# Kernel optimization log

Measured on AMD Instinct MI355X. Metric: run time of the kernel, lower is better.

The kernel has to match this reference:

```python
import jax, jax.numpy as jnp
import numpy as np

C = 2.0 + 1e-6
_nodes, _weights = np.polynomial.laguerre.laggauss(2)
QUAD_NODES = jnp.asarray(np.maximum(_nodes, 0.01) / C, dtype=jnp.float32)
QUAD_WEIGHTS = jnp.asarray(np.maximum(_weights, 0.01) / C, dtype=jnp.float32)
H, HD, P, M = 4, 64, 16, 32  # heads, head_dim, poly_dim, num_features
NUM_LABELS = 131072


def safe_normalize(x, axis=-1, eps=1e-4):
    n = jnp.linalg.norm(x, axis=axis, keepdims=True)
    return x / jnp.maximum(n, eps)


def safe_log(x, eps=1e-8):
    return jnp.log(jnp.maximum(x, eps))


def slay_features(x, omega, anchors):
    # x: [N, H*HD]; omega: [R,H,HD,M] (pre-scaled); anchors: [P,HD] (unit-norm)
    N = x.shape[0]
    xr = safe_normalize(x.reshape(N, H, HD), axis=-1)
    poly_proj = jnp.clip(jnp.einsum('nhd,pd->nhp', xr, anchors), -1.0, 1.0)
    poly_feat = poly_proj ** 2 / np.float32(np.sqrt(P))          # [N,H,P]
    prf_proj = jnp.einsum('nhd,rhdm->rnhm', xr, omega)           # [R,N,H,M]
    s = jnp.maximum(QUAD_NODES, 1e-6).reshape(-1, 1, 1, 1)
    exp_arg = jnp.clip(prf_proj * jnp.sqrt(2.0 * s) - s, -20.0, 20.0)
    prf_feat = jnp.exp(exp_arg) / np.float32(np.sqrt(M + 1e-6))
    prf_feat = prf_feat * jnp.sqrt(jnp.maximum(QUAD_WEIGHTS, 1e-6)).reshape(-1, 1, 1, 1)
    # fuse poly x prf, concat over quadrature nodes r (r-major feature order)
    fused = poly_feat[None, :, :, :, None] * prf_feat[:, :, :, None, :]  # [R,N,H,P,M]
    return fused.transpose(1, 0, 2, 3, 4).reshape(N, -1)         # [N, R*H*P*M]


def setup_inputs() -> dict:
    key = jax.random.key(0)
    ks = jax.random.split(key, 9)
    B, L, K = 1024, 128, 8
    return {
        'indices': jax.random.randint(ks[0], (B, L), 0, 100000),
        'mask': jnp.ones((B, L), dtype=jnp.float32),
        'labels': jax.random.randint(ks[1], (B, K), 0, NUM_LABELS),
        'label_mask': jnp.ones((B, K), dtype=jnp.float32),
        'neg_indices': jax.random.randint(ks[2], (2048,), 0, NUM_LABELS),
        'embed_table': jax.random.normal(ks[3], (100000, 256), dtype=jnp.float32),
        'kernel': jax.random.normal(ks[4], (256, NUM_LABELS), dtype=jnp.float32),
        'omega': jax.random.normal(ks[5], (2, H, HD, M), dtype=jnp.float32),
        'anchors': jax.random.normal(ks[6], (P, HD), dtype=jnp.float32),
    }


def reference(indices, mask, labels, label_mask, neg_indices, embed_table, kernel, omega, anchors):
    B, K = labels.shape
    # init-time parameter normalizations from the module
    omega_n = omega / np.float32(np.sqrt(HD))
    anchors_n = anchors / jnp.linalg.norm(anchors, axis=-1, keepdims=True)
    # MeanEmbedding encoder
    embeds = embed_table[indices]                                 # [B,L,D]
    summed = jnp.sum(embeds * mask[:, :, None], axis=1)
    query = summed / jnp.maximum(jnp.sum(mask, axis=1, keepdims=True), 1.0)
    query = safe_normalize(query, axis=-1)
    phi_query = slay_features(query, omega_n, anchors_n)          # [B,F]
    # sampled classifier rows
    W = safe_normalize(kernel.T, axis=-1)                         # [num_labels,D]
    safe_labels = jnp.maximum(labels, 0)
    all_needed = jnp.concatenate([safe_labels.reshape(-1), neg_indices])  # [B*K+Nneg]
    W_subset = W[all_needed]
    phi_W = slay_features(W_subset, omega_n, anchors_n)           # [B*K+Nneg,F]
    scores = phi_query @ phi_W.T                                  # [B, B*K+Nneg]
    idx_offsets = jnp.arange(B)[:, None] * K + jnp.arange(K)[None, :]
    pos_scores = jnp.take_along_axis(scores, idx_offsets, axis=1) # [B,K]
    neg_scores = scores[:, B * K:]                                # [B,Nneg]
    all_scores = jnp.concatenate([pos_scores, neg_scores], axis=1) + 1e-8
    log_Z = jax.scipy.special.logsumexp(safe_log(all_scores), axis=1)
    log_probs = safe_log(pos_scores + 1e-8) - log_Z[:, None]
    return -jnp.sum(log_probs * label_mask) / (jnp.sum(label_mask) + 1e-6)
```

## Files before the change

kernel.cpp:

```cpp
#include <hip/hip_runtime.h>
#include <math.h>

#define B_Q 1024
#define L_SEQ 128
#define D_EMB 256
#define NLAB 131072
#define LBL_ROWS 8192
#define NEG_ROWS 2048
#define W_ROWS 10240
#define CROW 320
#define RPB 32
#define SXS 258
#define QST 84
#define NWT 32

__device__ __forceinline__ float wave_sum(float v) {
#pragma unroll
  for (int off = 32; off > 0; off >>= 1) v += __shfl_xor(v, off, 64);
  return v;
}

__device__ __forceinline__ void slay_tail(const float* __restrict__ sx, int t,
                                          const float* __restrict__ anchT,
                                          const float* __restrict__ omega,
                                          float* __restrict__ outrow) {
  if (t < 64) {
    const int h = t >> 4, p = t & 15;
    const float* x = sx + h * 64;
    float d = 0.f;
#pragma unroll
    for (int dd = 0; dd < 64; dd++) d = fmaf(x[dd], anchT[dd * 16 + p], d);
    d = fminf(fmaxf(d, -1.0f), 1.0f);
    outrow[h * 16 + p] = d * d * 0.25f;
  }
  {
    const int r = t >> 7;
    const int h = (t >> 5) & 3;
    const float* x = sx + h * 64;
    const float* om = omega + (size_t)(t >> 5) * 2048 + (t & 31);
    float d = 0.f;
#pragma unroll
    for (int dd = 0; dd < 64; dd++) d = fmaf(x[dd], om[dd * 32], d);
    const float proj = d * 0.125f;
    const float s = r ? 1.70710592763316f : 0.29289307236691f;
    const float w = r ? 0.07322326809171f : 0.42677648190829f;
    float arg = proj * sqrtf(2.0f * s) - s;
    arg = fminf(fmaxf(arg, -20.0f), 20.0f);
    outrow[64 + t] = expf(arg) * (sqrtf(w) / sqrtf(32.000001f));
  }
}

__global__ __launch_bounds__(256) void k_setup(const float* __restrict__ anchors,
                                               const int* __restrict__ labels,
                                               const int* __restrict__ negidx,
                                               float* __restrict__ anchT,
                                               int* __restrict__ jidx,
                                               int* __restrict__ sorted) {
  __shared__ int shist[2048];
  __shared__ int s2[256];
  const int t = threadIdx.x, bx = blockIdx.x;
  if (bx == 0) {
    if (t < 64) {
      for (int p = 0; p < 16; p++) {
        const float v = anchors[p * 64 + t];
        const float n = sqrtf(wave_sum(v * v));
        anchT[t * 16 + p] = v / n;
      }
    }
  } else {
    for (int i = t; i < 2048; i += 256) shist[i] = 0;
    __syncthreads();
    int4 lv[8], nv[2];
#pragma unroll
    for (int e = 0; e < 8; e++) {
      int4 v = ((const int4*)labels)[e * 256 + t];
      v.x = max(v.x, 0); v.y = max(v.y, 0); v.z = max(v.z, 0); v.w = max(v.w, 0);
      lv[e] = v;
      ((int4*)jidx)[e * 256 + t] = v;
      atomicAdd(&shist[v.x >> 6], 1); atomicAdd(&shist[v.y >> 6], 1);
      atomicAdd(&shist[v.z >> 6], 1); atomicAdd(&shist[v.w >> 6], 1);
    }
#pragma unroll
    for (int e = 0; e < 2; e++) {
      const int4 v = ((const int4*)negidx)[e * 256 + t];
      nv[e] = v;
      ((int4*)jidx)[2048 + e * 256 + t] = v;
      atomicAdd(&shist[v.x >> 6], 1); atomicAdd(&shist[v.y >> 6], 1);
      atomicAdd(&shist[v.z >> 6], 1); atomicAdd(&shist[v.w >> 6], 1);
    }
    __syncthreads();
    int v[8]; int sum = 0;
#pragma unroll
    for (int e = 0; e < 8; e++) { v[e] = shist[t * 8 + e]; sum += v[e]; }
    s2[t] = sum; __syncthreads();
    for (int off = 1; off < 256; off <<= 1) {
      const int x = s2[t];
      const int y = (t >= off) ? s2[t - off] : 0;
      __syncthreads();
      s2[t] = x + y;
      __syncthreads();
    }
    int run = s2[t] - sum;
#pragma unroll
    for (int e = 0; e < 8; e++) { shist[t * 8 + e] = run; run += v[e]; }
    __syncthreads();
#pragma unroll
    for (int e = 0; e < 8; e++) {
      const int i = (e * 256 + t) * 4;
      sorted[atomicAdd(&shist[lv[e].x >> 6], 1)] = i;
      sorted[atomicAdd(&shist[lv[e].y >> 6], 1)] = i + 1;
      sorted[atomicAdd(&shist[lv[e].z >> 6], 1)] = i + 2;
      sorted[atomicAdd(&shist[lv[e].w >> 6], 1)] = i + 3;
    }
#pragma unroll
    for (int e = 0; e < 2; e++) {
      const int i = LBL_ROWS + (e * 256 + t) * 4;
      sorted[atomicAdd(&shist[nv[e].x >> 6], 1)] = i;
      sorted[atomicAdd(&shist[nv[e].y >> 6], 1)] = i + 1;
      sorted[atomicAdd(&shist[nv[e].z >> 6], 1)] = i + 2;
      sorted[atomicAdd(&shist[nv[e].w >> 6], 1)] = i + 3;
    }
  }
}

__global__ __launch_bounds__(256, 4) void k_feat(const int* __restrict__ indices,
                                                 const float* __restrict__ mask,
                                                 const float* __restrict__ embed,
                                                 const float* __restrict__ kern,
                                                 const float* __restrict__ anchT,
                                                 const float* __restrict__ omega,
                                                 const int* __restrict__ jidx,
                                                 const int* __restrict__ sorted,
                                                 float* __restrict__ qcomp,
                                                 float* __restrict__ wcomp) {
  __shared__ __align__(16) float smem[9504];
  const int tid = threadIdx.x;

  if (blockIdx.x < B_Q) {
    const int b = blockIdx.x, t = tid;
    const int wv = t >> 6, ln = t & 63;
    int* sidx = (int*)smem;
    float* smask = smem + 128;
    float4* spart = (float4*)(smem + 256);
    float* smsum = smem + 1280;
    float* sx = smem + 1296;
    if (t < L_SEQ) { sidx[t] = indices[b * L_SEQ + t]; smask[t] = mask[b * L_SEQ + t]; }
    __syncthreads();
    float4 acc = {0.f, 0.f, 0.f, 0.f};
    float msum = 0.f;
#pragma unroll 8
    for (int l = wv * 32; l < wv * 32 + 32; l++) {
      const float m = smask[l];
      msum += m;
      const float4 e = *(const float4*)(embed + (size_t)sidx[l] * D_EMB + ln * 4);
      acc.x = fmaf(e.x, m, acc.x); acc.y = fmaf(e.y, m, acc.y);
      acc.z = fmaf(e.z, m, acc.z); acc.w = fmaf(e.w, m, acc.w);
    }
    spart[wv * 64 + ln] = acc;
    if (ln == 0) smsum[wv] = msum;
    __syncthreads();
    const float* spf = (const float*)spart;
    float q = spf[t] + spf[256 + t] + spf[512 + t] + spf[768 + t];
    const float mt = smsum[0] + smsum[1] + smsum[2] + smsum[3];
    q /= fmaxf(mt, 1.0f);
    const float ss = wave_sum(q * q);
    sx[t] = q / fmaxf(sqrtf(ss), 1e-4f);
    __syncthreads();
    slay_tail(sx, t, anchT, omega, qcomp + (size_t)b * CROW);
  } else {
    const int lb = blockIdx.x - B_Q;
    int* sj = (int*)smem;
    int* ssid = (int*)smem + 32;
    float* rnorm = smem + 64;
    float* sq = smem + 192;
    float* sx = smem + 1248;
    const int cb = (lb & 7) * 40 + (lb >> 3);
    const int i0 = cb * RPB;

    if (tid < RPB) {
      const int sid = sorted[i0 + tid];
      ssid[tid] = sid;
      sj[tid] = jidx[sid];
    }
    __syncthreads();

    {
      const int row = tid & 31, dloc = tid >> 5;
      const float* kbase = kern + ((size_t)dloc << 17) + (size_t)sj[row];
      float ssq[4] = {0.f, 0.f, 0.f, 0.f};
#pragma unroll
      for (int it = 0; it < 32; it++) {
        const float v = kbase[(size_t)it << 20];
        sx[row * SXS + it * 8 + dloc] = v;
        ssq[it >> 3] = fmaf(v, v, ssq[it >> 3]);
      }
#pragma unroll
      for (int h = 0; h < 4; h++) sq[row * 33 + dloc * 4 + h] = ssq[h];
    }
    __syncthreads();
    if (tid < 128) {
      const int r2 = tid >> 2, h = tid & 3;
      float s = 0.f;
#pragma unroll
      for (int dl = 0; dl < 8; dl++) s += sq[r2 * 33 + dl * 4 + h];
      rnorm[r2 * 4 + h] = 1.0f / fmaxf(sqrtf(s), 1e-4f);
    }
    __syncthreads();

    {
      const int hh = (tid >> 5) & 3, r = tid >> 7;
      const float* om = omega + (size_t)(tid >> 5) * 2048 + (tid & 31);
      const float s = r ? 1.70710592763316f : 0.29289307236691f;
      const float w = r ? 0.07322326809171f : 0.42677648190829f;
      const float sc = sqrtf(2.0f * s);
      const float outs = sqrtf(w) / sqrtf(32.000001f);
#pragma unroll
      for (int half = 0; half < 2; half++) {
        float acc[16];
#pragma unroll
        for (int rq = 0; rq < 16; rq++) acc[rq] = 0.f;
#pragma unroll
        for (int dd = 0; dd < 64; dd += 2) {
          const float o0 = om[dd * 32], o1 = om[dd * 32 + 32];
#pragma unroll
          for (int rq = 0; rq < 16; rq++) {
            const float2 xv = *(const float2*)(sx + (half * 16 + rq) * SXS + hh * 64 + dd);
            acc[rq] = fmaf(xv.x, o0, fmaf(xv.y, o1, acc[rq]));
          }
        }
#pragma unroll
        for (int rq = 0; rq < 16; rq++) {
          const int row = half * 16 + rq;
          float arg = acc[rq] * 0.125f * rnorm[row * 4 + hh] * sc - s;
          arg = fminf(fmaxf(arg, -20.0f), 20.0f);
          wcomp[(size_t)ssid[row] * CROW + 64 + tid] = expf(arg) * outs;
        }
      }
    }

    {
      const int hp = tid & 63, rp = tid >> 6;
      const int h = hp >> 4, p = hp & 15;
#pragma unroll
      for (int pr = 0; pr < 4; pr++) {
        const int r0 = rp * 8 + pr * 2;
        const float* x0 = sx + r0 * SXS + h * 64;
        const float* x1 = x0 + SXS;
        float d0 = 0.f, d1 = 0.f;
#pragma unroll
        for (int dd = 0; dd < 64; dd++) {
          const float a = anchT[dd * 16 + p];
          d0 = fmaf(x0[dd], a, d0);
          d1 = fmaf(x1[dd], a, d1);
        }
        d0 *= rnorm[r0 * 4 + h];
        d1 *= rnorm[(r0 + 1) * 4 + h];
        d0 = fminf(fmaxf(d0, -1.0f), 1.0f);
        d1 = fminf(fmaxf(d1, -1.0f), 1.0f);
        wcomp[(size_t)ssid[r0] * CROW + h * 16 + p]     = d0 * d0 * 0.25f;
        wcomp[(size_t)ssid[r0 + 1] * CROW + h * 16 + p] = d1 * d1 * 0.25f;
      }
    }
  }
}

__global__ __launch_bounds__(256) void k_score(const float* __restrict__ qcomp,
                                               const float* __restrict__ wcomp,
                                               float* __restrict__ negparts,
                                               float* __restrict__ pos) {
  __shared__ __align__(16) float sq[128 * QST];
  __shared__ __align__(16) float swt[80 * 64];
  const int tid = threadIdx.x;

  if (blockIdx.x < 256) {
    const int qt = blockIdx.x & 7;
    const int wb = blockIdx.x >> 3;
    const int q0 = qt * 128;
    const int wr0 = LBL_ROWS + wb * 64;
    const int qg = tid >> 4;
    const int wg = tid & 15;

    float acc[8][4];
#pragma unroll
    for (int i = 0; i < 8; i++)
#pragma unroll
      for (int j = 0; j < 4; j++) acc[i][j] = 0.f;

    for (int h = 0; h < 4; h++) {
#pragma unroll
      for (int k = 0; k < 10; k++) {
        const int idx = k * 256 + tid;
        const int row = idx / 20, c4 = idx % 20;
        int col;
        if (c4 < 4)       col = h * 16 + c4 * 4;
        else if (c4 < 12) col = 64 + h * 32 + (c4 - 4) * 4;
        else              col = 192 + h * 32 + (c4 - 12) * 4;
        const float4 v = *(const float4*)(qcomp + (size_t)(q0 + row) * CROW + col);
        *(float4*)(sq + row * QST + c4 * 4) = v;
      }
#pragma unroll
      for (int k = 0; k < 5; k++) {
        const int idx = k * 256 + tid;
        const int row = idx / 20, c4 = idx % 20;
        int col;
        if (c4 < 4)       col = h * 16 + c4 * 4;
        else if (c4 < 12) col = 64 + h * 32 + (c4 - 4) * 4;
        else              col = 192 + h * 32 + (c4 - 12) * 4;
        const float4 v = *(const float4*)(wcomp + (size_t)(wr0 + row) * CROW + col);
        swt[(c4 * 4 + 0) * 64 + row] = v.x;
        swt[(c4 * 4 + 1) * 64 + row] = v.y;
        swt[(c4 * 4 + 2) * 64 + row] = v.z;
        swt[(c4 * 4 + 3) * 64 + row] = v.w;
      }
      __syncthreads();

      float pd[8][4], pf[8][4];
#pragma unroll
      for (int i = 0; i < 8; i++)
#pragma unroll
        for (int j = 0; j < 4; j++) { pd[i][j] = 0.f; pf[i][j] = 0.f; }

#pragma unroll
      for (int c = 0; c < 20; c++) {
        float4 qv[8];
#pragma unroll
        for (int i = 0; i < 8; i++)
          qv[i] = *(const float4*)(sq + (qg * 8 + i) * QST + c * 4);
#pragma unroll
        for (int k = 0; k < 4; k++) {
          const float4 wvk = *(const float4*)(swt + (c * 4 + k) * 64 + wg * 4);
          if (c < 4) {
#pragma unroll
            for (int i = 0; i < 8; i++) {
              const float qik = ((const float*)&qv[i])[k];
              pd[i][0] = fmaf(qik, wvk.x, pd[i][0]);
              pd[i][1] = fmaf(qik, wvk.y, pd[i][1]);
              pd[i][2] = fmaf(qik, wvk.z, pd[i][2]);
              pd[i][3] = fmaf(qik, wvk.w, pd[i][3]);
            }
          } else {
#pragma unroll
            for (int i = 0; i < 8; i++) {
              const float qik = ((const float*)&qv[i])[k];
              pf[i][0] = fmaf(qik, wvk.x, pf[i][0]);
              pf[i][1] = fmaf(qik, wvk.y, pf[i][1]);
              pf[i][2] = fmaf(qik, wvk.z, pf[i][2]);
              pf[i][3] = fmaf(qik, wvk.w, pf[i][3]);
            }
          }
        }
      }
#pragma unroll
      for (int i = 0; i < 8; i++)
#pragma unroll
        for (int j = 0; j < 4; j++) acc[i][j] = fmaf(pd[i][j], pf[i][j], acc[i][j]);
      __syncthreads();
    }

#pragma unroll
    for (int i = 0; i < 8; i++) {
      float r = acc[i][0] + acc[i][1] + acc[i][2] + acc[i][3];
      r += __shfl_xor(r, 1, 64);
      r += __shfl_xor(r, 2, 64);
      r += __shfl_xor(r, 4, 64);
      r += __shfl_xor(r, 8, 64);
      if (wg == 0) negparts[wb * B_Q + q0 + qg * 8 + i] = r;
    }
  } else {
    const int g = (blockIdx.x - 256) * 64 + (tid >> 2);
    const int h = tid & 3;
    const float* q = qcomp + (size_t)(g >> 3) * CROW;
    const float* w = wcomp + (size_t)g * CROW;
    float pd = 0.f, pf = 0.f;
#pragma unroll
    for (int c = 0; c < 4; c++) {
      const float4 qv = *(const float4*)(q + h * 16 + c * 4);
      const float4 wv = *(const float4*)(w + h * 16 + c * 4);
      pd += qv.x * wv.x + qv.y * wv.y + qv.z * wv.z + qv.w * wv.w;
    }
#pragma unroll
    for (int r = 0; r < 2; r++)
#pragma unroll
      for (int c = 0; c < 8; c++) {
        const float4 qv = *(const float4*)(q + 64 + r * 128 + h * 32 + c * 4);
        const float4 wv = *(const float4*)(w + 64 + r * 128 + h * 32 + c * 4);
        pf += qv.x * wv.x + qv.y * wv.y + qv.z * wv.z + qv.w * wv.w;
      }
    float sc = pd * pf;
    sc += __shfl_xor(sc, 1, 64);
    sc += __shfl_xor(sc, 2, 64);
    if (h == 0) pos[g] = sc;
  }
}

__global__ __launch_bounds__(1024) void k_loss(const float* __restrict__ pos,
                                               const float* __restrict__ negparts,
                                               const float* __restrict__ lmask,
                                               float* __restrict__ out) {
  const int b = threadIdx.x;
  float lp[8];
  float possum = 0.f;
#pragma unroll
  for (int k = 0; k < 8; k++) { lp[k] = pos[b * 8 + k]; possum += lp[k]; }
  float negsum = 0.f;
#pragma unroll 8
  for (int c = 0; c < NWT; c++) negsum += negparts[c * B_Q + b];
  const float Z = possum + negsum + 2.056e-5f;
  const float logZ = logf(Z);
  float local = 0.f, lsum = 0.f;
#pragma unroll
  for (int k = 0; k < 8; k++) {
    const float lm = lmask[b * 8 + k];
    local += lm * (logf(lp[k] + 1e-8f) - logZ);
    lsum += lm;
  }
  local = wave_sum(local);
  lsum = wave_sum(lsum);
  __shared__ float r1[16], r2[16];
  const int wid = b >> 6;
  if ((b & 63) == 0) { r1[wid] = local; r2[wid] = lsum; }
  __syncthreads();
  if (b == 0) {
    float t1 = 0.f, t2 = 0.f;
    for (int wv = 0; wv < 16; wv++) { t1 += r1[wv]; t2 += r2[wv]; }
    out[0] = -t1 / (t2 + 1e-6f);
  }
}

extern "C" void kernel_launch(void* const* d_in, const int* in_sizes, int n_in,
                              void* d_out, int out_size, void* d_ws, size_t ws_size,
                              hipStream_t stream) {
  const int* indices  = (const int*)d_in[0];
  const float* mask   = (const float*)d_in[1];
  const int* labels   = (const int*)d_in[2];
  const float* lmask  = (const float*)d_in[3];
  const int* negidx   = (const int*)d_in[4];
  const float* embed  = (const float*)d_in[5];
  const float* kern   = (const float*)d_in[6];
  const float* omega  = (const float*)d_in[7];
  const float* anchors= (const float*)d_in[8];
  float* out = (float*)d_out;

  float* ws = (float*)d_ws;
  float* anchT    = ws;
  float* qcomp    = anchT + 1024;
  float* wcomp    = qcomp + (size_t)B_Q * CROW;
  float* pos      = wcomp + (size_t)W_ROWS * CROW;
  float* negparts = pos + LBL_ROWS;
  int*   jidx     = (int*)(negparts + NWT * B_Q);
  int*   sorted   = jidx + W_ROWS;

  k_setup<<<2, 256, 0, stream>>>(anchors, labels, negidx, anchT, jidx, sorted);
  k_feat<<<B_Q + W_ROWS / RPB, 256, 0, stream>>>(indices, mask, embed, kern, anchT, omega,
                                                 jidx, sorted, qcomp, wcomp);
  k_score<<<256 + 128, 256, 0, stream>>>(qcomp, wcomp, negparts, pos);
  k_loss<<<1, 1024, 0, stream>>>(pos, negparts, lmask, out);
}
```

Measured before the change: 357.1 us.

## Shrink W-feature blocks to 8 rows and schedule them before query blocks

The classifier-row feature path now processes 8 gathered rows per block instead of 32, giving 1280 smaller blocks with far less shared memory. Each thread loads one embedding dimension for all 8 rows, and row norms come from wave reductions instead of a shared partial-sum pass. The W blocks are also launched ahead of the query-embedding blocks. The aim is higher occupancy and more memory parallelism for the strided column gather from the kernel matrix. The cost is that the omega and anchor loads are reused across fewer rows per block.

```diff
diff --git a/kernel.cpp b/kernel.cpp
--- a/kernel.cpp
+++ b/kernel.cpp
@@ -9,7 +9,8 @@
 #define NEG_ROWS 2048
 #define W_ROWS 10240
 #define CROW 320
-#define RPB 32
+#define RPB 8
+#define NWB 1280
 #define SXS 258
 #define QST 84
 #define NWT 32
@@ -123,21 +124,98 @@
   }
 }
 
-__global__ __launch_bounds__(256, 4) void k_feat(const int* __restrict__ indices,
-                                                 const float* __restrict__ mask,
-                                                 const float* __restrict__ embed,
-                                                 const float* __restrict__ kern,
-                                                 const float* __restrict__ anchT,
-                                                 const float* __restrict__ omega,
-                                                 const int* __restrict__ jidx,
-                                                 const int* __restrict__ sorted,
-                                                 float* __restrict__ qcomp,
-                                                 float* __restrict__ wcomp) {
-  __shared__ __align__(16) float smem[9504];
+__global__ __launch_bounds__(256) void k_feat(const int* __restrict__ indices,
+                                              const float* __restrict__ mask,
+                                              const float* __restrict__ embed,
+                                              const float* __restrict__ kern,
+                                              const float* __restrict__ anchT,
+                                              const float* __restrict__ omega,
+                                              const int* __restrict__ jidx,
+                                              const int* __restrict__ sorted,
+                                              float* __restrict__ qcomp,
+                                              float* __restrict__ wcomp) {
+  __shared__ __align__(16) float smem[2112];
   const int tid = threadIdx.x;
 
-  if (blockIdx.x < B_Q) {
-    const int b = blockIdx.x, t = tid;
+  if (blockIdx.x < NWB) {
+    const int lb = blockIdx.x;
+    int* sj = (int*)smem;
+    int* ssid = (int*)smem + 8;
+    float* rnorm = smem + 16;
+    float* sx = smem + 48;
+    const int cb = (lb & 7) * 160 + (lb >> 3);
+    const int i0 = cb * RPB;
+
+    if (tid < RPB) {
+      const int sid = sorted[i0 + tid];
+      ssid[tid] = sid;
+      sj[tid] = jidx[sid];
+    }
+    __syncthreads();
+
+    {
+      const float* kbase = kern + ((size_t)tid << 17);
+      float vv[8];
+#pragma unroll
+      for (int k = 0; k < RPB; k++) vv[k] = kbase[sj[k]];
+#pragma unroll
+      for (int k = 0; k < RPB; k++) {
+        sx[k * SXS + tid] = vv[k];
+        const float ss = wave_sum(vv[k] * vv[k]);
+        if ((tid & 63) == 0) rnorm[k * 4 + (tid >> 6)] = 1.0f / fmaxf(sqrtf(ss), 1e-4f);
+      }
+    }
+    __syncthreads();
+
+    {
+      const int hh = (tid >> 5) & 3, r = tid >> 7;
+      const float* om = omega + (size_t)(tid >> 5) * 2048 + (tid & 31);
+      const float s = r ? 1.70710592763316f : 0.29289307236691f;
+      const float w = r ? 0.07322326809171f : 0.42677648190829f;
+      const float sc = sqrtf(2.0f * s);
+      const float outs = sqrtf(w) / sqrtf(32.000001f);
+      float acc[RPB];
+#pragma unroll
+      for (int k = 0; k < RPB; k++) acc[k] = 0.f;
+#pragma unroll
+      for (int dd = 0; dd < 64; dd += 2) {
+        const float o0 = om[dd * 32], o1 = om[dd * 32 + 32];
+#pragma unroll
+        for (int k = 0; k < RPB; k++) {
+          const float2 xv = *(const float2*)(sx + k * SXS + hh * 64 + dd);
+          acc[k] = fmaf(xv.x, o0, fmaf(xv.y, o1, acc[k]));
+        }
+      }
+#pragma unroll
+      for (int k = 0; k < RPB; k++) {
+        float arg = acc[k] * 0.125f * rnorm[k * 4 + hh] * sc - s;
+        arg = fminf(fmaxf(arg, -20.0f), 20.0f);
+        wcomp[(size_t)ssid[k] * CROW + 64 + tid] = expf(arg) * outs;
+      }
+    }
+
+    {
+      const int hp = tid & 63, rp = tid >> 6;
+      const int h = hp >> 4, p = hp & 15;
+      const int r0 = rp * 2;
+      const float* x0 = sx + r0 * SXS + h * 64;
+      const float* x1 = x0 + SXS;
+      float d0 = 0.f, d1 = 0.f;
+#pragma unroll
+      for (int dd = 0; dd < 64; dd++) {
+        const float a = anchT[dd * 16 + p];
+        d0 = fmaf(x0[dd], a, d0);
+        d1 = fmaf(x1[dd], a, d1);
+      }
+      d0 *= rnorm[r0 * 4 + h];
+      d1 *= rnorm[(r0 + 1) * 4 + h];
+      d0 = fminf(fmaxf(d0, -1.0f), 1.0f);
+      d1 = fminf(fmaxf(d1, -1.0f), 1.0f);
+      wcomp[(size_t)ssid[r0] * CROW + h * 16 + p]     = d0 * d0 * 0.25f;
+      wcomp[(size_t)ssid[r0 + 1] * CROW + h * 16 + p] = d1 * d1 * 0.25f;
+    }
+  } else {
+    const int b = blockIdx.x - NWB, t = tid;
     const int wv = t >> 6, ln = t & 63;
     int* sidx = (int*)smem;
     float* smask = smem + 128;
@@ -167,100 +245,6 @@
     sx[t] = q / fmaxf(sqrtf(ss), 1e-4f);
     __syncthreads();
     slay_tail(sx, t, anchT, omega, qcomp + (size_t)b * CROW);
-  } else {
-    const int lb = blockIdx.x - B_Q;
-    int* sj = (int*)smem;
-    int* ssid = (int*)smem + 32;
-    float* rnorm = smem + 64;
-    float* sq = smem + 192;
-    float* sx = smem + 1248;
-    const int cb = (lb & 7) * 40 + (lb >> 3);
-    const int i0 = cb * RPB;
-
-    if (tid < RPB) {
-      const int sid = sorted[i0 + tid];
-      ssid[tid] = sid;
-      sj[tid] = jidx[sid];
-    }
-    __syncthreads();
-
-    {
-      const int row = tid & 31, dloc = tid >> 5;
-      const float* kbase = kern + ((size_t)dloc << 17) + (size_t)sj[row];
-      float ssq[4] = {0.f, 0.f, 0.f, 0.f};
-#pragma unroll
-      for (int it = 0; it < 32; it++) {
-        const float v = kbase[(size_t)it << 20];
-        sx[row * SXS + it * 8 + dloc] = v;
-        ssq[it >> 3] = fmaf(v, v, ssq[it >> 3]);
-      }
-#pragma unroll
-      for (int h = 0; h < 4; h++) sq[row * 33 + dloc * 4 + h] = ssq[h];
-    }
-    __syncthreads();
-    if (tid < 128) {
-      const int r2 = tid >> 2, h = tid & 3;
-      float s = 0.f;
-#pragma unroll
-      for (int dl = 0; dl < 8; dl++) s += sq[r2 * 33 + dl * 4 + h];
-      rnorm[r2 * 4 + h] = 1.0f / fmaxf(sqrtf(s), 1e-4f);
-    }
-    __syncthreads();
-
-    {
-      const int hh = (tid >> 5) & 3, r = tid >> 7;
-      const float* om = omega + (size_t)(tid >> 5) * 2048 + (tid & 31);
-      const float s = r ? 1.70710592763316f : 0.29289307236691f;
-      const float w = r ? 0.07322326809171f : 0.42677648190829f;
-      const float sc = sqrtf(2.0f * s);
-      const float outs = sqrtf(w) / sqrtf(32.000001f);
-#pragma unroll
-      for (int half = 0; half < 2; half++) {
-        float acc[16];
-#pragma unroll
-        for (int rq = 0; rq < 16; rq++) acc[rq] = 0.f;
-#pragma unroll
-        for (int dd = 0; dd < 64; dd += 2) {
-          const float o0 = om[dd * 32], o1 = om[dd * 32 + 32];
-#pragma unroll
-          for (int rq = 0; rq < 16; rq++) {
-            const float2 xv = *(const float2*)(sx + (half * 16 + rq) * SXS + hh * 64 + dd);
-            acc[rq] = fmaf(xv.x, o0, fmaf(xv.y, o1, acc[rq]));
-          }
-        }
-#pragma unroll
-        for (int rq = 0; rq < 16; rq++) {
-          const int row = half * 16 + rq;
-          float arg = acc[rq] * 0.125f * rnorm[row * 4 + hh] * sc - s;
-          arg = fminf(fmaxf(arg, -20.0f), 20.0f);
-          wcomp[(size_t)ssid[row] * CROW + 64 + tid] = expf(arg) * outs;
-        }
-      }
-    }
-
-    {
-      const int hp = tid & 63, rp = tid >> 6;
-      const int h = hp >> 4, p = hp & 15;
-#pragma unroll
-      for (int pr = 0; pr < 4; pr++) {
-        const int r0 = rp * 8 + pr * 2;
-        const float* x0 = sx + r0 * SXS + h * 64;
-        const float* x1 = x0 + SXS;
-        float d0 = 0.f, d1 = 0.f;
-#pragma unroll
-        for (int dd = 0; dd < 64; dd++) {
-          const float a = anchT[dd * 16 + p];
-          d0 = fmaf(x0[dd], a, d0);
-          d1 = fmaf(x1[dd], a, d1);
-        }
-        d0 *= rnorm[r0 * 4 + h];
-        d1 *= rnorm[(r0 + 1) * 4 + h];
-        d0 = fminf(fmaxf(d0, -1.0f), 1.0f);
-        d1 = fminf(fmaxf(d1, -1.0f), 1.0f);
-        wcomp[(size_t)ssid[r0] * CROW + h * 16 + p]     = d0 * d0 * 0.25f;
-        wcomp[(size_t)ssid[r0 + 1] * CROW + h * 16 + p] = d1 * d1 * 0.25f;
-      }
-    }
   }
 }
 
@@ -451,8 +435,8 @@
   int*   sorted   = jidx + W_ROWS;
 
   k_setup<<<2, 256, 0, stream>>>(anchors, labels, negidx, anchT, jidx, sorted);
-  k_feat<<<B_Q + W_ROWS / RPB, 256, 0, stream>>>(indices, mask, embed, kern, anchT, omega,
-                                                 jidx, sorted, qcomp, wcomp);
+  k_feat<<<NWB + B_Q, 256, 0, stream>>>(indices, mask, embed, kern, anchT, omega,
+                                        jidx, sorted, qcomp, wcomp);
   k_score<<<256 + 128, 256, 0, stream>>>(qcomp, wcomp, negparts, pos);
   k_loss<<<1, 1024, 0, stream>>>(pos, negparts, lmask, out);
 }
```

New measurement: 338.8 us. -5.1%, faster.
